# Performance work log

Measured on AMD Instinct MI355X. Metric: run time of the kernel, lower is better.

## Reference

```python
import jax, jax.numpy as jnp
import numpy as np

V, E, CIN, COUT, NH, HID = 8192, 2048, 128, 128, 4, 32
EPS = 1e-5

def _ln(x, g, b):
    m = x.mean(-1, keepdims=True)
    v = x.var(-1, keepdims=True)
    return (x - m) / jnp.sqrt(v + EPS) * g + b

def setup_inputs() -> dict:
    key = jax.random.key(0)
    ks = jax.random.split(key, 12)
    s = 0.05
    X = jax.random.normal(ks[0], (V, CIN), jnp.float32)
    H = jax.random.bernoulli(ks[1], 0.02, (V, E)).astype(jnp.float32)
    edge_features = jax.random.normal(ks[2], (E, COUT), jnp.float32)
    Wv = jax.random.normal(ks[3], (CIN, COUT), jnp.float32) * s
    bv = jnp.zeros((COUT,), jnp.float32)
    We = jax.random.normal(ks[4], (COUT, COUT), jnp.float32) * s
    be = jnp.zeros((COUT,), jnp.float32)
    vW1 = jax.random.normal(ks[5], (NH, CIN, HID), jnp.float32) * s
    vb1 = jnp.zeros((NH, HID), jnp.float32)
    vW2 = jax.random.normal(ks[6], (NH, HID), jnp.float32) * s
    vb2 = jnp.zeros((NH,), jnp.float32)
    eW1 = jax.random.normal(ks[7], (COUT, HID), jnp.float32) * s
    eb1 = jnp.zeros((HID,), jnp.float32)
    eW2 = jax.random.normal(ks[8], (HID,), jnp.float32) * s
    eb2 = jnp.zeros((), jnp.float32)
    Wc = jax.random.normal(ks[9], (NH * COUT, COUT), jnp.float32) * s
    bc = jnp.zeros((COUT,), jnp.float32)
    Wg = jax.random.normal(ks[10], (CIN + COUT, COUT), jnp.float32) * s
    bg = jnp.zeros((COUT,), jnp.float32)
    return dict(X=X, H=H, edge_features=edge_features, Wv=Wv, bv=bv, We=We, be=be,
                vW1=vW1, vb1=vb1, vW2=vW2, vb2=vb2, eW1=eW1, eb1=eb1, eW2=eW2, eb2=eb2,
                Wc=Wc, bc=bc,
                ln_e_g=jnp.ones((COUT,), jnp.float32), ln_e_b=jnp.zeros((COUT,), jnp.float32),
                ln_v_g=jnp.ones((COUT,), jnp.float32), ln_v_b=jnp.zeros((COUT,), jnp.float32),
                bn_g=jnp.ones((COUT,), jnp.float32), bn_b=jnp.zeros((COUT,), jnp.float32),
                Wg=Wg, bg=bg)

def reference(X, H, edge_features, Wv, bv, We, be, vW1, vb1, vW2, vb2,
              eW1, eb1, eW2, eb2, Wc, bc, ln_e_g, ln_e_b, ln_v_g, ln_v_b,
              bn_g, bn_b, Wg, bg):
    gelu = lambda t: jax.nn.gelu(t, approximate=False)  # torch nn.GELU default (erf)
    Ht = H.T                                   # (E, V)
    Xt = X @ Wv + bv                           # (V, Cout) theta_v
    # per-head vertex attention MLP: Linear(Cin,32)->GELU->Linear(32,1), vectorized over heads
    hid = gelu(jnp.einsum('vc,hck->hvk', X, vW1) + vb1[:, None, :])
    attn = jax.nn.sigmoid(jnp.einsum('hvk,hk->hv', hid, vW2) + vb2[:, None])  # (NH, V)
    deg = Ht.sum(axis=1, keepdims=True)        # (E, 1) edge degrees
    denom = jnp.maximum(deg, 1.0)
    # degree-normalized attention-weighted v2e aggregation per head
    head_e = jnp.einsum('ev,hvc->hec', Ht, Xt[None] * attn[:, :, None]) / denom[None]
    e_cat = jnp.transpose(head_e, (1, 0, 2)).reshape(E, NH * COUT)  # concat heads dim=1
    e_feat = e_cat @ Wc + bc                   # attn_combine
    # edge attention uses the LAST head's vertex weights (global-var quirk in torch code)
    edge_att = ((Ht @ attn[-1]) / jnp.maximum(deg[:, 0], 1.0))[:, None]  # (E,1)
    # edge-feature gating with e_attention head 0
    te = edge_features @ We + be               # theta_e
    e_scores = gelu(e_feat @ eW1 + eb1) @ eW2 + eb2
    ew = jax.nn.sigmoid(e_scores)[:, None]
    e_feat = e_feat * ew + te * (1.0 - ew)
    # normalize == 'both': layer_norm_e then batch_norm (training-mode batch stats)
    e_feat = _ln(e_feat, ln_e_g, ln_e_b)
    m = e_feat.mean(axis=0)
    v = e_feat.var(axis=0)
    e_feat = (e_feat - m) / jnp.sqrt(v + EPS) * bn_g + bn_b
    # e2v sum aggregation: H @ e_feat
    v_feat = H @ e_feat                        # (V, Cout)
    gate = jax.nn.sigmoid(jnp.concatenate([X, v_feat], axis=1) @ Wg + bg)
    v_feat = gate * v_feat + (1.0 - gate) * Xt
    v_feat = _ln(v_feat, ln_v_g, ln_v_b)
    v_feat = v_feat + X                        # residual (Cin == Cout)
    v_feat = gelu(v_feat)                      # not is_last: activation; dropout = identity (eval)
    e_feat = gelu(e_feat)
    return v_feat, e_feat, edge_att
```

## Files before the change

kernel.cpp:

```cpp
#include <hip/hip_runtime.h>
#include <hip/hip_bf16.h>
#include <math.h>

#define NV 8192
#define NE 2048
#define CIN 128
#define COUT 128
#define NH 4
#define HID 32
#define ETILE 8
#define LCAP 256
#define VCAP 96
#define NWORDS (NE / 64)
#define TWORDS (NV / 64)
#define EPSV 1e-5f

__device__ __forceinline__ float gelu_f(float x) {
    return 0.5f * x * (1.0f + erff(x * 0.70710678118654752f));
}
__device__ __forceinline__ float sigmoid_f(float x) {
    return 1.0f / (1.0f + expf(-x));
}

__global__ __launch_bounds__(256) void k_front(
    const float* __restrict__ X, const float* __restrict__ Wv, const float* __restrict__ bv,
    const float* __restrict__ vW1, const float* __restrict__ vb1,
    const float* __restrict__ vW2, const float* __restrict__ vb2,
    const float* __restrict__ H,
    float* __restrict__ Xt, float* __restrict__ attn4,
    unsigned long long* __restrict__ Hbits, int* __restrict__ vdeg, int* __restrict__ vlist)
{
    __shared__ float Xs[2][8][CIN];
    int t = threadIdx.x;
    if (blockIdx.x < NV / 16) {
        int half = t >> 7, tt = t & 127;
        int v0 = blockIdx.x * 16 + half * 8;
        for (int v = 0; v < 8; ++v) Xs[half][v][tt] = X[(size_t)(v0 + v) * CIN + tt];
        __syncthreads();

        float acc[8];
        float bvc = bv[tt];
#pragma unroll
        for (int v = 0; v < 8; ++v) acc[v] = bvc;
        for (int k = 0; k < CIN; ++k) {
            float w = Wv[k * COUT + tt];
#pragma unroll
            for (int v = 0; v < 8; ++v) acc[v] = fmaf(Xs[half][v][k], w, acc[v]);
        }
        for (int v = 0; v < 8; ++v) Xt[(size_t)(v0 + v) * COUT + tt] = acc[v];

        int h = tt >> 5, j = tt & 31;
        float hb = vb1[h * HID + j];
#pragma unroll
        for (int v = 0; v < 8; ++v) acc[v] = hb;
        for (int k = 0; k < CIN; ++k) {
            float w = vW1[(h * CIN + k) * HID + j];
#pragma unroll
            for (int v = 0; v < 8; ++v) acc[v] = fmaf(Xs[half][v][k], w, acc[v]);
        }
        float w2 = vW2[h * HID + j];
        float b2 = vb2[h];
        for (int v = 0; v < 8; ++v) {
            float val = gelu_f(acc[v]) * w2;
#pragma unroll
            for (int m = 16; m >= 1; m >>= 1) val += __shfl_xor(val, m, 64);
            if (j == 0) attn4[(size_t)(v0 + v) * NH + h] = sigmoid_f(val + b2);
        }
    } else {
        int b = blockIdx.x - NV / 16;
        int w = t >> 6;
        int lane = t & 63;
        int v = b * 4 + w;
        const float4* row4 = (const float4*)(H + (size_t)v * NE);
        int base = 0;
        int* vl = vlist + (size_t)v * VCAP;
#pragma unroll
        for (int it = 0; it < NE / 1024; ++it) {
            int e0 = it * 1024 + lane * 16;
            float4 f0 = row4[it * 256 + lane * 4 + 0];
            float4 f1 = row4[it * 256 + lane * 4 + 1];
            float4 f2 = row4[it * 256 + lane * 4 + 2];
            float4 f3 = row4[it * 256 + lane * 4 + 3];
            unsigned int m16 = 0;
            m16 |= (f0.x != 0.0f ? 1u : 0u) << 0;  m16 |= (f0.y != 0.0f ? 1u : 0u) << 1;
            m16 |= (f0.z != 0.0f ? 1u : 0u) << 2;  m16 |= (f0.w != 0.0f ? 1u : 0u) << 3;
            m16 |= (f1.x != 0.0f ? 1u : 0u) << 4;  m16 |= (f1.y != 0.0f ? 1u : 0u) << 5;
            m16 |= (f1.z != 0.0f ? 1u : 0u) << 6;  m16 |= (f1.w != 0.0f ? 1u : 0u) << 7;
            m16 |= (f2.x != 0.0f ? 1u : 0u) << 8;  m16 |= (f2.y != 0.0f ? 1u : 0u) << 9;
            m16 |= (f2.z != 0.0f ? 1u : 0u) << 10; m16 |= (f2.w != 0.0f ? 1u : 0u) << 11;
            m16 |= (f3.x != 0.0f ? 1u : 0u) << 12; m16 |= (f3.y != 0.0f ? 1u : 0u) << 13;
            m16 |= (f3.z != 0.0f ? 1u : 0u) << 14; m16 |= (f3.w != 0.0f ? 1u : 0u) << 15;

            int cnt = __popc(m16);
            int inc = cnt;
#pragma unroll
            for (int s = 1; s < 64; s <<= 1) {
                int y = __shfl_up(inc, s, 64);
                if (lane >= s) inc += y;
            }
            int tot = __shfl(inc, 63, 64);
            int q = lane & 15;
            unsigned int w0 = __shfl(m16, q * 4 + 0, 64);
            unsigned int w1 = __shfl(m16, q * 4 + 1, 64);
            unsigned int w2 = __shfl(m16, q * 4 + 2, 64);
            unsigned int w3 = __shfl(m16, q * 4 + 3, 64);
            if (lane < 16) {
                unsigned long long word = (unsigned long long)w0
                    | ((unsigned long long)w1 << 16)
                    | ((unsigned long long)w2 << 32)
                    | ((unsigned long long)w3 << 48);
                Hbits[(size_t)v * NWORDS + it * 16 + lane] = word;
            }
            int off = base + inc - cnt;
            unsigned int mm = m16;
            while (mm) {
                int j = __ffs(mm) - 1;
                mm &= mm - 1;
                if (off < VCAP) vl[off] = e0 + j;
                ++off;
            }
            base += tot;
        }
        if (lane == 0) vdeg[v] = base;
    }
}

__global__ __launch_bounds__(256) void k_transpose(
    const unsigned long long* __restrict__ Hbits, unsigned long long* __restrict__ HbitsT)
{
    __shared__ unsigned long long rows[64][NWORDS];
    int t = threadIdx.x;
    int vt = blockIdx.x;
    for (int i = t; i < 64 * NWORDS; i += 256)
        rows[i >> 5][i & 31] = Hbits[(size_t)vt * 64 * NWORDS + i];
    __syncthreads();
    int wv = t >> 6;
    int lane = t & 63;
    const unsigned long long M[6] = {
        0xFFFFFFFF00000000ULL, 0xFFFF0000FFFF0000ULL, 0xFF00FF00FF00FF00ULL,
        0xF0F0F0F0F0F0F0F0ULL, 0xCCCCCCCCCCCCCCCCULL, 0xAAAAAAAAAAAAAAAAULL };
    const int js[6] = {32, 16, 8, 4, 2, 1};
#pragma unroll
    for (int itb = 0; itb < 8; ++itb) {
        int it = wv * 8 + itb;
        unsigned long long x = rows[lane][it];
#pragma unroll
        for (int s = 0; s < 6; ++s) {
            int j = js[s];
            unsigned long long y = __shfl_xor(x, j, 64);
            unsigned long long Ms = M[s];
            if ((lane & j) == 0) x = (x & ~Ms) | ((y << j) & Ms);
            else                 x = (x & Ms) | ((y >> j) & ~Ms);
        }
        HbitsT[(size_t)(it * 64 + lane) * TWORDS + vt] = x;
    }
}

__global__ __launch_bounds__(256) void k_agg(
    const float* __restrict__ Xt, const float* __restrict__ attn4,
    const unsigned long long* __restrict__ HbitsT,
    float* __restrict__ ecat_g, float* __restrict__ out_att)
{
    __shared__ int lst[LCAP];
    __shared__ int wsum[2];
    __shared__ float pt[4][NH][COUT];
    __shared__ float asp[4];

    int t = threadIdx.x;
    int wid = t >> 6, lane = t & 63;
    int e = blockIdx.x;

    unsigned long long wd = 0ull;
    if (t < 128) wd = HbitsT[(size_t)e * TWORDS + t];
    int cnt = __popcll(wd);
    int inc = cnt;
#pragma unroll
    for (int s = 1; s < 64; s <<= 1) {
        int y = __shfl_up(inc, s, 64);
        if (lane >= s) inc += y;
    }
    if (lane == 63 && wid < 2) wsum[wid] = inc;
    __syncthreads();
    int n0 = wsum[0] + wsum[1];
    if (t < 128) {
        int base = (wid ? wsum[0] : 0) + inc - cnt;
        int vbase = t * 64;
        unsigned long long mm = wd;
        while (mm) {
            int i = __ffsll(mm) - 1;
            mm &= mm - 1;
            if (base < LCAP) lst[base] = vbase + i;
            ++base;
        }
    }
    __syncthreads();

    float inv = 1.0f / fmaxf((float)n0, 1.0f);
    int n = n0 < LCAP ? n0 : LCAP;

    float p00 = 0, p10 = 0, p20 = 0, p30 = 0;
    float p01 = 0, p11 = 0, p21 = 0, p31 = 0;
    float as = 0;
#pragma unroll 2
    for (int i = wid; i < n; i += 4) {
        int v = lst[i];
        float x0 = Xt[(size_t)v * COUT + lane];
        float x1 = Xt[(size_t)v * COUT + lane + 64];
        float4 a = *(const float4*)(attn4 + (size_t)v * NH);
        p00 = fmaf(x0, a.x, p00);  p01 = fmaf(x1, a.x, p01);
        p10 = fmaf(x0, a.y, p10);  p11 = fmaf(x1, a.y, p11);
        p20 = fmaf(x0, a.z, p20);  p21 = fmaf(x1, a.z, p21);
        p30 = fmaf(x0, a.w, p30);  p31 = fmaf(x1, a.w, p31);
        as += a.w;
    }
    pt[wid][0][lane] = p00;  pt[wid][0][lane + 64] = p01;
    pt[wid][1][lane] = p10;  pt[wid][1][lane + 64] = p11;
    pt[wid][2][lane] = p20;  pt[wid][2][lane + 64] = p21;
    pt[wid][3][lane] = p30;  pt[wid][3][lane + 64] = p31;
    if (lane == 0) asp[wid] = as;
    __syncthreads();

#pragma unroll
    for (int r = 0; r < 2; ++r) {
        int k = t + r * 256;
        int h = k >> 7, ch = k & 127;
        float s = pt[0][h][ch] + pt[1][h][ch] + pt[2][h][ch] + pt[3][h][ch];
        ecat_g[(size_t)e * 512 + k] = s * inv;
    }
    if (t == 0) out_att[e] = (asp[0] + asp[1] + asp[2] + asp[3]) * inv;
}

__global__ __launch_bounds__(512) void k_combine(
    const float* __restrict__ ecat_g, const float* __restrict__ edge_features,
    const float* __restrict__ Wc, const float* __restrict__ bc,
    const float* __restrict__ We, const float* __restrict__ be,
    const float* __restrict__ eW1, const float* __restrict__ eb1,
    const float* __restrict__ eW2, const float* __restrict__ eb2,
    const float* __restrict__ ln_g, const float* __restrict__ ln_b,
    float* __restrict__ e_ln, float* __restrict__ bn_sum, float* __restrict__ bn_sq)
{
    __shared__ float ecs[ETILE][512];
    __shared__ float efr[ETILE][COUT];
    __shared__ float efs[ETILE][COUT];
    __shared__ float teL[ETILE][COUT];
    __shared__ float yb[ETILE][COUT];
    __shared__ float ews[ETILE];
    __shared__ float red[ETILE][2][2];

    int t = threadIdx.x;
    int e0 = blockIdx.x * ETILE;
    int eslot = t >> 7, c = t & 127;
    int lane = t & 63;
    int gw = (t >> 6) & 1;

    for (int idx = t; idx < ETILE * 512; idx += 512)
        ecs[idx >> 9][idx & 511] = ecat_g[(size_t)e0 * 512 + idx];
    for (int idx = t; idx < ETILE * COUT; idx += 512)
        efr[idx >> 7][idx & 127] = edge_features[(size_t)e0 * COUT + idx];
    __syncthreads();

    float accW0 = 0, accW1 = 0;
    for (int k = 0; k < 512; ++k) {
        float w = Wc[(size_t)k * COUT + c];
        accW0 = fmaf(ecs[eslot][k], w, accW0);
        accW1 = fmaf(ecs[eslot + 4][k], w, accW1);
    }
    float accT0 = 0, accT1 = 0;
    for (int k = 0; k < COUT; ++k) {
        float w = We[(size_t)k * COUT + c];
        accT0 = fmaf(efr[eslot][k], w, accT0);
        accT1 = fmaf(efr[eslot + 4][k], w, accT1);
    }
    float bcc = bc[c], bec = be[c];
    efs[eslot][c] = accW0 + bcc;
    efs[eslot + 4][c] = accW1 + bcc;
    teL[eslot][c] = accT0 + bec;
    teL[eslot + 4][c] = accT1 + bec;
    __syncthreads();

    if (t < ETILE * 32) {
        int ee = t >> 5, j = t & 31;
        float hj = eb1[j];
        for (int k = 0; k < COUT; ++k) hj = fmaf(efs[ee][k], eW1[k * HID + j], hj);
        float val = gelu_f(hj) * eW2[j];
#pragma unroll
        for (int m = 16; m >= 1; m >>= 1) val += __shfl_xor(val, m, 32);
        if (j == 0) ews[ee] = sigmoid_f(val + eb2[0]);
    }
    __syncthreads();

#pragma unroll
    for (int j = 0; j < 2; ++j) {
        int e = eslot + 4 * j;
        float ew = ews[e];
        float x = efs[e][c] * ew + teL[e][c] * (1.0f - ew);
        float s = x, q = x * x;
#pragma unroll
        for (int m = 32; m >= 1; m >>= 1) { s += __shfl_xor(s, m, 64); q += __shfl_xor(q, m, 64); }
        if (lane == 0) { red[e][gw][0] = s; red[e][gw][1] = q; }
        __syncthreads();
        float S = red[e][0][0] + red[e][1][0];
        float Q = red[e][0][1] + red[e][1][1];
        float m_ = S * (1.0f / COUT);
        float var = Q * (1.0f / COUT) - m_ * m_;
        float y = (x - m_) * rsqrtf(var + EPSV) * ln_g[c] + ln_b[c];
        e_ln[(size_t)(e0 + e) * COUT + c] = y;
        yb[e][c] = y;
        __syncthreads();
    }

    if (t < 128) {
        float s = 0, q = 0;
#pragma unroll
        for (int e = 0; e < ETILE; ++e) { float y = yb[e][t]; s += y; q += y * y; }
        atomicAdd(&bn_sum[t], s);
        atomicAdd(&bn_sq[t], q);
    }
}

__global__ __launch_bounds__(256) void k_bnapply(const float* __restrict__ e_ln,
    const float* __restrict__ bn_sum, const float* __restrict__ bn_sq,
    const float* __restrict__ bn_g, const float* __restrict__ bn_b,
    float* __restrict__ out_e)
{
    int idx = blockIdx.x * 256 + threadIdx.x;
    int c = idx & 127;
    float m = bn_sum[c] * (1.0f / NE);
    float var = bn_sq[c] * (1.0f / NE) - m * m;
    float x = e_ln[idx];
    float y = (x - m) * rsqrtf(var + EPSV) * bn_g[c] + bn_b[c];
    out_e[idx] = gelu_f(y);
}

__global__ __launch_bounds__(512) void k_vertex2(
    const float* __restrict__ X, const int* __restrict__ vdeg, const int* __restrict__ vlist,
    const float* __restrict__ e_ln,
    const float* __restrict__ bn_sum, const float* __restrict__ bn_sq,
    const float* __restrict__ bn_g, const float* __restrict__ bn_b,
    const float* __restrict__ Xt,
    const float* __restrict__ Wg, const float* __restrict__ bg,
    const float* __restrict__ ln_g, const float* __restrict__ ln_b,
    float* __restrict__ out_v)
{
    __shared__ float XsF[8 * CIN];
    __shared__ float vfF[8 * COUT];
    __shared__ int lst[8][VCAP];
    __shared__ int degs[8];
    __shared__ float part[4 * 8 * COUT];
    __shared__ float red[8][2][2];

    int t = threadIdx.x;
    int vg = t >> 6, lane = t & 63;
    int g4 = t >> 7, c = t & 127;
    int gw2 = (t >> 6) & 1;
    int v0 = blockIdx.x * 8;

    {
        float2 x2 = *(const float2*)(X + (size_t)(v0 + vg) * CIN + lane * 2);
        XsF[vg * CIN + lane * 2] = x2.x;
        XsF[vg * CIN + lane * 2 + 1] = x2.y;
    }
    for (int i = t; i < 8 * VCAP; i += 512)
        lst[i / VCAP][i % VCAP] = vlist[(size_t)v0 * VCAP + i];
    if (t < 8) degs[t] = vdeg[v0 + t];
    __syncthreads();

    int ch0 = lane * 2;
    float m0 = bn_sum[ch0] * (1.0f / NE);
    float m1 = bn_sum[ch0 + 1] * (1.0f / NE);
    float A0 = bn_g[ch0] * rsqrtf(bn_sq[ch0] * (1.0f / NE) - m0 * m0 + EPSV);
    float A1 = bn_g[ch0 + 1] * rsqrtf(bn_sq[ch0 + 1] * (1.0f / NE) - m1 * m1 + EPSV);
    float B0 = bn_b[ch0] - m0 * A0;
    float B1 = bn_b[ch0 + 1] - m1 * A1;

    int n = degs[vg];
    if (n > VCAP) n = VCAP;
    float sx = 0, sy = 0;
    for (int i = 0; i < n; ++i) {
        float2 v2 = *(const float2*)(e_ln + (size_t)lst[vg][i] * COUT + ch0);
        sx += v2.x;
        sy += v2.y;
    }
    float fn = (float)n;
    vfF[vg * COUT + ch0] = A0 * sx + fn * B0;
    vfF[vg * COUT + ch0 + 1] = A1 * sy + fn * B1;
    __syncthreads();

    {
        float accW[8] = {0, 0, 0, 0, 0, 0, 0, 0};
        const float* wp = Wg + (size_t)(g4 * 64) * COUT + c;
        const float* src = (g4 < 2) ? XsF : vfF;
        int kb = (g4 & 1) * 64;
        for (int ki = 0; ki < 64; ++ki) {
            float w = wp[(size_t)ki * COUT];
#pragma unroll
            for (int v = 0; v < 8; ++v)
                accW[v] = fmaf(src[v * 128 + kb + ki], w, accW[v]);
        }
#pragma unroll
        for (int v = 0; v < 8; ++v) part[g4 * 1024 + v * COUT + c] = accW[v];
    }
    __syncthreads();

    float xv[2];
#pragma unroll
    for (int rep = 0; rep < 2; ++rep) {
        int v = g4 + rep * 4;
        float ag = part[0 * 1024 + v * COUT + c] + part[1 * 1024 + v * COUT + c]
                 + part[2 * 1024 + v * COUT + c] + part[3 * 1024 + v * COUT + c] + bg[c];
        float gate = sigmoid_f(ag);
        float x = gate * vfF[v * COUT + c] + (1.0f - gate) * Xt[(size_t)(v0 + v) * COUT + c];
        xv[rep] = x;
        float s = x, q = x * x;
#pragma unroll
        for (int m = 32; m >= 1; m >>= 1) { s += __shfl_xor(s, m, 64); q += __shfl_xor(q, m, 64); }
        if (lane == 0) { red[v][gw2][0] = s; red[v][gw2][1] = q; }
    }
    __syncthreads();
#pragma unroll
    for (int rep = 0; rep < 2; ++rep) {
        int v = g4 + rep * 4;
        float S = red[v][0][0] + red[v][1][0];
        float Q = red[v][0][1] + red[v][1][1];
        float m_ = S * (1.0f / COUT);
        float var = Q * (1.0f / COUT) - m_ * m_;
        float y = (xv[rep] - m_) * rsqrtf(var + EPSV) * ln_g[c] + ln_b[c];
        y = y + XsF[v * CIN + c];
        out_v[(size_t)(v0 + v) * COUT + c] = gelu_f(y);
    }
}

extern "C" void kernel_launch(void* const* d_in, const int* in_sizes, int n_in,
                              void* d_out, int out_size, void* d_ws, size_t ws_size,
                              hipStream_t stream) {
    const float* X    = (const float*)d_in[0];
    const float* H    = (const float*)d_in[1];
    const float* edge_features = (const float*)d_in[2];
    const float* Wv   = (const float*)d_in[3];
    const float* bv   = (const float*)d_in[4];
    const float* We   = (const float*)d_in[5];
    const float* be   = (const float*)d_in[6];
    const float* vW1  = (const float*)d_in[7];
    const float* vb1  = (const float*)d_in[8];
    const float* vW2  = (const float*)d_in[9];
    const float* vb2  = (const float*)d_in[10];
    const float* eW1  = (const float*)d_in[11];
    const float* eb1  = (const float*)d_in[12];
    const float* eW2  = (const float*)d_in[13];
    const float* eb2  = (const float*)d_in[14];
    const float* Wc   = (const float*)d_in[15];
    const float* bc   = (const float*)d_in[16];
    const float* ln_e_g = (const float*)d_in[17];
    const float* ln_e_b = (const float*)d_in[18];
    const float* ln_v_g = (const float*)d_in[19];
    const float* ln_v_b = (const float*)d_in[20];
    const float* bn_g = (const float*)d_in[21];
    const float* bn_b = (const float*)d_in[22];
    const float* Wg   = (const float*)d_in[23];
    const float* bg   = (const float*)d_in[24];

    float* out_v  = (float*)d_out;
    float* out_e  = out_v + NV * COUT;
    float* out_att = out_e + NE * COUT;

    char* w = (char*)d_ws;
    float* Xt     = (float*)w; w += (size_t)NV * COUT * 4;
    float* attn4  = (float*)w; w += (size_t)NV * NH * 4;
    float* e_ln   = (float*)w; w += (size_t)NE * COUT * 4;
    float* ecat_g = (float*)w; w += (size_t)NE * NH * COUT * 4;
    float* bn_sum = (float*)w; w += COUT * 4;
    float* bn_sq  = (float*)w; w += COUT * 4;
    int*   vdeg   = (int*)w;   w += (size_t)NV * 4;
    int*   vlist  = (int*)w;   w += (size_t)NV * VCAP * 4;
    unsigned long long* Hbits  = (unsigned long long*)w; w += (size_t)NV * NWORDS * 8;
    unsigned long long* HbitsT = (unsigned long long*)w; w += (size_t)NE * TWORDS * 8;

    hipMemsetAsync(bn_sum, 0, 2 * COUT * sizeof(float), stream);

    k_front<<<NV / 16 + NV / 4, 256, 0, stream>>>(X, Wv, bv, vW1, vb1, vW2, vb2, H,
                                                  Xt, attn4, Hbits, vdeg, vlist);
    k_transpose<<<NV / 64, 256, 0, stream>>>(Hbits, HbitsT);
    k_agg<<<NE, 256, 0, stream>>>(Xt, attn4, HbitsT, ecat_g, out_att);
    k_combine<<<NE / ETILE, 512, 0, stream>>>(ecat_g, edge_features,
                                              Wc, bc, We, be, eW1, eb1, eW2, eb2,
                                              ln_e_g, ln_e_b, e_ln, bn_sum, bn_sq);
    k_bnapply<<<(NE * COUT) / 256, 256, 0, stream>>>(e_ln, bn_sum, bn_sq, bn_g, bn_b, out_e);
    k_vertex2<<<NV / 8, 512, 0, stream>>>(X, vdeg, vlist, e_ln, bn_sum, bn_sq, bn_g, bn_b,
                                          Xt, Wg, bg, ln_v_g, ln_v_b, out_v);
}
```

Before: 269.5 us.

## Split combine GEMMs into K-split partial kernel plus reduction kernel

The edge combine matmuls (ecat×Wc and edge_features×We) move out of the single per-tile kernel into a new kernel. It splits the reduction dimension four ways across blocks and two ways within each block, and each thread keeps 8 edge accumulators so every weight load is reused eight times. A second kernel sums the four partial slices, adds the biases, and then runs the original gating, layer-norm and batch-stat logic. This gives 1024 blocks instead of 256 and more weight reuse per load. The cost is an extra launch and writing then reading 8 MB of partial sums in global memory.

```diff
diff --git a/kernel.cpp b/kernel.cpp
--- a/kernel.cpp
+++ b/kernel.cpp
@@ -230,17 +230,83 @@
     if (t == 0) out_att[e] = (asp[0] + asp[1] + asp[2] + asp[3]) * inv;
 }
 
-__global__ __launch_bounds__(512) void k_combine(
+__global__ __launch_bounds__(256) void k_cpart(
     const float* __restrict__ ecat_g, const float* __restrict__ edge_features,
-    const float* __restrict__ Wc, const float* __restrict__ bc,
-    const float* __restrict__ We, const float* __restrict__ be,
+    const float* __restrict__ Wc, const float* __restrict__ We,
+    float* __restrict__ efp, float* __restrict__ tep)
+{
+    __shared__ float ecs[ETILE][128];
+    __shared__ float efr8[ETILE][32];
+    __shared__ float part[2][ETILE][128];
+
+    int t = threadIdx.x;
+    int s = blockIdx.x & 3;
+    int eb = blockIdx.x >> 2;
+    int e0 = eb * ETILE;
+    int c = t & 127, h = t >> 7;
+
+    for (int idx = t; idx < ETILE * 128; idx += 256) {
+        int e = idx >> 7, k = idx & 127;
+        ecs[e][k] = ecat_g[(size_t)(e0 + e) * 512 + s * 128 + k];
+    }
+    if (t < ETILE * 32) {
+        int e = t >> 5, k = t & 31;
+        efr8[e][k] = edge_features[(size_t)(e0 + e) * COUT + s * 32 + k];
+    }
+    __syncthreads();
+
+    float accW[ETILE] = {0, 0, 0, 0, 0, 0, 0, 0};
+    {
+        const float* wp = Wc + (size_t)(s * 128 + h * 64) * COUT + c;
+        for (int kk = 0; kk < 64; ++kk) {
+            float w = wp[(size_t)kk * COUT];
+            int k = h * 64 + kk;
+#pragma unroll
+            for (int e = 0; e < ETILE; ++e)
+                accW[e] = fmaf(ecs[e][k], w, accW[e]);
+        }
+    }
+#pragma unroll
+    for (int e = 0; e < ETILE; ++e) part[h][e][c] = accW[e];
+    __syncthreads();
+    if (h == 0) {
+#pragma unroll
+        for (int e = 0; e < ETILE; ++e)
+            efp[(size_t)s * NE * COUT + (size_t)(e0 + e) * COUT + c] =
+                part[0][e][c] + part[1][e][c];
+    }
+    __syncthreads();
+
+    float accT[ETILE] = {0, 0, 0, 0, 0, 0, 0, 0};
+    {
+        const float* wt = We + (size_t)(s * 32 + h * 16) * COUT + c;
+        for (int kk = 0; kk < 16; ++kk) {
+            float w = wt[(size_t)kk * COUT];
+            int k = h * 16 + kk;
+#pragma unroll
+            for (int e = 0; e < ETILE; ++e)
+                accT[e] = fmaf(efr8[e][k], w, accT[e]);
+        }
+    }
+#pragma unroll
+    for (int e = 0; e < ETILE; ++e) part[h][e][c] = accT[e];
+    __syncthreads();
+    if (h == 0) {
+#pragma unroll
+        for (int e = 0; e < ETILE; ++e)
+            tep[(size_t)s * NE * COUT + (size_t)(e0 + e) * COUT + c] =
+                part[0][e][c] + part[1][e][c];
+    }
+}
+
+__global__ __launch_bounds__(512) void k_cred(
+    const float* __restrict__ efp, const float* __restrict__ tep,
+    const float* __restrict__ bc, const float* __restrict__ be,
     const float* __restrict__ eW1, const float* __restrict__ eb1,
     const float* __restrict__ eW2, const float* __restrict__ eb2,
     const float* __restrict__ ln_g, const float* __restrict__ ln_b,
     float* __restrict__ e_ln, float* __restrict__ bn_sum, float* __restrict__ bn_sq)
 {
-    __shared__ float ecs[ETILE][512];
-    __shared__ float efr[ETILE][COUT];
     __shared__ float efs[ETILE][COUT];
     __shared__ float teL[ETILE][COUT];
     __shared__ float yb[ETILE][COUT];
@@ -253,29 +319,19 @@
     int lane = t & 63;
     int gw = (t >> 6) & 1;
 
-    for (int idx = t; idx < ETILE * 512; idx += 512)
-        ecs[idx >> 9][idx & 511] = ecat_g[(size_t)e0 * 512 + idx];
-    for (int idx = t; idx < ETILE * COUT; idx += 512)
-        efr[idx >> 7][idx & 127] = edge_features[(size_t)e0 * COUT + idx];
-    __syncthreads();
-
-    float accW0 = 0, accW1 = 0;
-    for (int k = 0; k < 512; ++k) {
-        float w = Wc[(size_t)k * COUT + c];
-        accW0 = fmaf(ecs[eslot][k], w, accW0);
-        accW1 = fmaf(ecs[eslot + 4][k], w, accW1);
-    }
-    float accT0 = 0, accT1 = 0;
-    for (int k = 0; k < COUT; ++k) {
-        float w = We[(size_t)k * COUT + c];
-        accT0 = fmaf(efr[eslot][k], w, accT0);
-        accT1 = fmaf(efr[eslot + 4][k], w, accT1);
-    }
-    float bcc = bc[c], bec = be[c];
-    efs[eslot][c] = accW0 + bcc;
-    efs[eslot + 4][c] = accW1 + bcc;
-    teL[eslot][c] = accT0 + bec;
-    teL[eslot + 4][c] = accT1 + bec;
+#pragma unroll
+    for (int j = 0; j < 2; ++j) {
+        int e = eslot + 4 * j;
+        size_t off = (size_t)(e0 + e) * COUT + c;
+        float ef = bc[c], te = be[c];
+#pragma unroll
+        for (int s = 0; s < 4; ++s) {
+            ef += efp[(size_t)s * NE * COUT + off];
+            te += tep[(size_t)s * NE * COUT + off];
+        }
+        efs[e][c] = ef;
+        teL[e][c] = te;
+    }
     __syncthreads();
 
     if (t < ETILE * 32) {
@@ -468,6 +524,8 @@
     float* attn4  = (float*)w; w += (size_t)NV * NH * 4;
     float* e_ln   = (float*)w; w += (size_t)NE * COUT * 4;
     float* ecat_g = (float*)w; w += (size_t)NE * NH * COUT * 4;
+    float* efp    = (float*)w; w += (size_t)4 * NE * COUT * 4;
+    float* tep    = (float*)w; w += (size_t)4 * NE * COUT * 4;
     float* bn_sum = (float*)w; w += COUT * 4;
     float* bn_sq  = (float*)w; w += COUT * 4;
     int*   vdeg   = (int*)w;   w += (size_t)NV * 4;
@@ -481,9 +539,9 @@
                                                   Xt, attn4, Hbits, vdeg, vlist);
     k_transpose<<<NV / 64, 256, 0, stream>>>(Hbits, HbitsT);
     k_agg<<<NE, 256, 0, stream>>>(Xt, attn4, HbitsT, ecat_g, out_att);
-    k_combine<<<NE / ETILE, 512, 0, stream>>>(ecat_g, edge_features,
-                                              Wc, bc, We, be, eW1, eb1, eW2, eb2,
-                                              ln_e_g, ln_e_b, e_ln, bn_sum, bn_sq);
+    k_cpart<<<(NE / ETILE) * 4, 256, 0, stream>>>(ecat_g, edge_features, Wc, We, efp, tep);
+    k_cred<<<NE / ETILE, 512, 0, stream>>>(efp, tep, bc, be, eW1, eb1, eW2, eb2,
+                                           ln_e_g, ln_e_b, e_ln, bn_sum, bn_sq);
     k_bnapply<<<(NE * COUT) / 256, 256, 0, stream>>>(e_ln, bn_sum, bn_sq, bn_g, bn_b, out_e);
     k_vertex2<<<NV / 8, 512, 0, stream>>>(X, vdeg, vlist, e_ln, bn_sum, bn_sq, bn_g, bn_b,
                                           Xt, Wg, bg, ln_v_g, ln_v_b, out_v);
```

New measurement: 258.4 us. -4.1%, faster.
